# Performance work log

Measured on AMD Instinct MI355X. Metric: run time of the kernel, lower is better.

## Reference

```python
import jax, jax.numpy as jnp
import numpy as np

B, C, T = 16, 512, 1024
C8 = C // 8


def setup_inputs() -> dict:
    key = jax.random.key(0)
    ks = jax.random.split(key, 8)
    s_in = 1.0 / np.sqrt(C)  # torch Conv1d default init scale (fan_in = C*1)
    x = jax.random.normal(ks[0], (B, C, T), dtype=jnp.float32)
    q_w = jax.random.uniform(ks[1], (C8, C), jnp.float32, -s_in, s_in)
    q_b = jax.random.uniform(ks[2], (C8,), jnp.float32, -s_in, s_in)
    k_w = jax.random.uniform(ks[3], (C8, C), jnp.float32, -s_in, s_in)
    k_b = jax.random.uniform(ks[4], (C8,), jnp.float32, -s_in, s_in)
    v_w = jax.random.uniform(ks[5], (C, C), jnp.float32, -s_in, s_in)
    v_b = jax.random.uniform(ks[6], (C,), jnp.float32, -s_in, s_in)
    # gamma is nn.Parameter(torch.zeros(1)) at init; use a nonzero value so the
    # attention branch actually contributes to the output/gradients.
    gamma = jnp.full((1,), 0.5, dtype=jnp.float32)
    return {"x": x, "q_w": q_w, "q_b": q_b, "k_w": k_w, "k_b": k_b,
            "v_w": v_w, "v_b": v_b, "gamma": gamma}


def reference(x, q_w, q_b, k_w, k_b, v_w, v_b, gamma):
    # 1x1 Conv1d == per-timestep linear: weight [out, in]
    q = jnp.einsum('bct,dc->btd', x, q_w) + q_b              # [B, T, C/8]
    k = jnp.einsum('bct,dc->bdt', x, k_w) + k_b[:, None]     # [B, C/8, T]
    energy = jnp.einsum('btd,bds->bts', q, k)                # [B, T, T]
    attn = jax.nn.softmax(energy, axis=-1)                   # softmax over keys s
    v = jnp.einsum('bct,dc->bdt', x, v_w) + v_b[:, None]     # [B, C, T]
    # out[b,c,t] = sum_s v[b,c,s] * attn[b,t,s]
    out = jnp.einsum('bcs,bts->bct', v, attn)                # [B, C, T]
    return gamma * out + x
```

## Files before the change

### kernel.cpp

```cpp
#include <hip/hip_runtime.h>
#include <math.h>

constexpr int Bc = 16;
constexpr int Cc = 512;
constexpr int Tc = 1024;

typedef unsigned short u16;
typedef __attribute__((ext_vector_type(8))) short bf16x8;
typedef __attribute__((ext_vector_type(4))) float floatx4;

__device__ inline u16 f2bf(float f) {
    union { float f; unsigned u; } v; v.f = f;
    unsigned r = v.u + 0x7FFFu + ((v.u >> 16) & 1u);
    return (u16)(r >> 16);
}

__device__ inline void async16(const void* g, void* l) {
    __builtin_amdgcn_global_load_lds(
        (const __attribute__((address_space(1))) unsigned*)g,
        (__attribute__((address_space(3))) unsigned*)l, 16, 0, 0);
}

__global__ __launch_bounds__(256) void wconv_kernel(
    const float* __restrict__ qw, const float* __restrict__ kw,
    const float* __restrict__ vw, u16* __restrict__ wb)
{
    int i4 = blockIdx.x * 256 + threadIdx.x;
    int e  = i4 * 4;
    int row = e >> 9, col = e & 511;
    const float* src = (row < 64)  ? qw + (size_t)row * 512 + col
                     : (row < 128) ? kw + (size_t)(row - 64) * 512 + col
                                   : vw + (size_t)(row - 128) * 512 + col;
    float4 v = *(const float4*)src;
    ushort4 o = { f2bf(v.x), f2bf(v.y), f2bf(v.z), f2bf(v.w) };
    *(ushort4*)(wb + e) = o;
}

__global__ __launch_bounds__(256) void xtrans_kernel(
    const float* __restrict__ x, u16* __restrict__ xt)
{
    const int b = blockIdx.z, c0 = blockIdx.y * 64, t0 = blockIdx.x * 64;
    const int tid = threadIdx.x;
    __shared__ float xs[64][65];

    const float* xb = x + ((size_t)(b * Cc + c0)) * Tc + t0;
    #pragma unroll
    for (int r = 0; r < 4; ++r) {
        int f = tid + 256 * r;
        int c = f >> 4, tf = f & 15;
        float4 v = *(const float4*)(xb + (size_t)c * Tc + tf * 4);
        xs[c][tf * 4 + 0] = v.x; xs[c][tf * 4 + 1] = v.y;
        xs[c][tf * 4 + 2] = v.z; xs[c][tf * 4 + 3] = v.w;
    }
    __syncthreads();
    u16* xo = xt + ((size_t)b * Tc + t0) * Cc + c0;
    #pragma unroll
    for (int r = 0; r < 4; ++r) {
        int t  = (tid >> 4) + 16 * r;
        int cc = tid & 15;
        ushort4 o;
        o.x = f2bf(xs[cc * 4 + 0][t]); o.y = f2bf(xs[cc * 4 + 1][t]);
        o.z = f2bf(xs[cc * 4 + 2][t]); o.w = f2bf(xs[cc * 4 + 3][t]);
        *(ushort4*)(xo + (size_t)t * Cc + cc * 4) = o;
    }
}

__global__ __launch_bounds__(256, 2) void proj_kernel(
    const u16* __restrict__ wb, const u16* __restrict__ xt,
    const float* __restrict__ qb, const float* __restrict__ kb,
    const float* __restrict__ vb,
    u16* __restrict__ qt, u16* __restrict__ kt, u16* __restrict__ vc)
{
    const int b   = blockIdx.z;
    const int t0  = blockIdx.x * 128;
    const int n0  = blockIdx.y * 128;
    const int tid = threadIdx.x;
    const int w = tid >> 6, lane = tid & 63;
    const int l15 = lane & 15, q = lane >> 4;
    const int r8 = lane >> 3, h = lane & 7;
    const int nh = w >> 1, th = w & 1;

    __shared__ u16 As[128 * 64];
    __shared__ u16 Bs[128 * 64];

    floatx4 acc[4][4];
    #pragma unroll
    for (int i = 0; i < 4; ++i)
        #pragma unroll
        for (int j = 0; j < 4; ++j) acc[i][j] = (floatx4){0.f, 0.f, 0.f, 0.f};

    const u16* wbase = wb + (size_t)n0 * Cc;
    const u16* xbase = xt + ((size_t)b * Tc + t0) * Cc;

    for (int k0 = 0; k0 < Cc; k0 += 64) {
        #pragma unroll
        for (int i = 0; i < 4; ++i) {
            int row  = w * 32 + i * 8 + r8;
            int gcol = k0 + (((h + row) & 7) << 3);
            async16(wbase + (size_t)row * Cc + gcol, &As[(w * 32 + i * 8) * 64]);
            async16(xbase + (size_t)row * Cc + gcol, &Bs[(w * 32 + i * 8) * 64]);
        }
        asm volatile("s_waitcnt vmcnt(0)" ::: "memory");
        __syncthreads();

        #pragma unroll
        for (int ko = 0; ko < 64; ko += 32) {
            bf16x8 af[4], bf[4];
            const int cc = (ko >> 3) + q;
            #pragma unroll
            for (int i = 0; i < 4; ++i) {
                int row = nh * 64 + i * 16 + l15;
                af[i] = *(const bf16x8*)&As[row * 64 + (((cc - row) & 7) << 3)];
            }
            #pragma unroll
            for (int j = 0; j < 4; ++j) {
                int row = th * 64 + j * 16 + l15;
                bf[j] = *(const bf16x8*)&Bs[row * 64 + (((cc - row) & 7) << 3)];
            }
            #pragma unroll
            for (int i = 0; i < 4; ++i)
                #pragma unroll
                for (int j = 0; j < 4; ++j)
                    acc[i][j] = __builtin_amdgcn_mfma_f32_16x16x32_bf16(
                        af[i], bf[j], acc[i][j], 0, 0, 0);
        }
        __syncthreads();
    }

    if (n0 >= 128) {
        const int c_base = n0 - 128 + nh * 64;
        u16* vbb = vc + (size_t)b * Cc * Tc;
        #pragma unroll
        for (int i = 0; i < 4; ++i) {
            #pragma unroll
            for (int rr = 0; rr < 4; ++rr) {
                int c = c_base + i * 16 + q * 4 + rr;
                float bias = vb[c];
                #pragma unroll
                for (int j = 0; j < 4; ++j) {
                    int t = t0 + th * 64 + j * 16 + l15;
                    vbb[((size_t)c << 10) + t] = f2bf(acc[i][j][rr] + bias);
                }
            }
        }
    } else {
        const float* bias_p = nh ? kb : qb;
        u16* dst = nh ? kt : qt;
        u16* reg = ((w & 2) ? Bs : As) + (w & 1) * 4096;
        #pragma unroll
        for (int jh = 0; jh < 2; ++jh) {
            #pragma unroll
            for (int j2 = 0; j2 < 2; ++j2) {
                int j = jh * 2 + j2;
                int t_loc = j2 * 16 + l15;
                #pragma unroll
                for (int i = 0; i < 4; ++i) {
                    ushort4 o;
                    float b0 = bias_p[i * 16 + q * 4 + 0];
                    float b1 = bias_p[i * 16 + q * 4 + 1];
                    float b2 = bias_p[i * 16 + q * 4 + 2];
                    float b3 = bias_p[i * 16 + q * 4 + 3];
                    o.x = f2bf(acc[i][j][0] + b0);
                    o.y = f2bf(acc[i][j][1] + b1);
                    o.z = f2bf(acc[i][j][2] + b2);
                    o.w = f2bf(acc[i][j][3] + b3);
                    *(ushort4*)&reg[t_loc * 72 + i * 16 + q * 4] = o;
                }
            }
            const int cc8 = lane & 7, tb = lane >> 3;
            #pragma unroll
            for (int rr2 = 0; rr2 < 4; ++rr2) {
                int t32 = tb * 4 + rr2;
                bf16x8 vv = *(const bf16x8*)&reg[t32 * 72 + cc8 * 8];
                int t = t0 + th * 64 + jh * 32 + t32;
                *(bf16x8*)(dst + ((size_t)b * Tc + t) * 64 + cc8 * 8) = vv;
            }
            __builtin_amdgcn_wave_barrier();
        }
    }
}

__global__ __launch_bounds__(256, 2) void attn_kernel(
    const float* __restrict__ x,
    const u16* __restrict__ qt, const u16* __restrict__ kt,
    const u16* __restrict__ vc, const float* __restrict__ gp,
    float* __restrict__ out)
{
    const int tid = threadIdx.x, lane = tid & 63, w = tid >> 6;
    const int l15 = lane & 15, q = lane >> 4;
    const int l    = blockIdx.x;
    const int xcd  = l & 7, slot = l >> 3;
    const int combo = xcd * 4 + (slot >> 4);
    const int bx = slot & 15;
    const int b  = combo >> 1;
    const int by = combo & 1;
    const int t0 = bx * 64;
    const int cb = by * 256;

    __shared__ u16   P[2][4][16][40];
    __shared__ float lrow[64];
    __shared__ float tr2[4][16][68];

    const u16* qp = qt + ((size_t)b * Tc + t0 + w * 16 + l15) * 64 + q * 8;
    const bf16x8 qf0 = *(const bf16x8*)qp;
    const bf16x8 qf1 = *(const bf16x8*)(qp + 32);

    const u16* ktb = kt + (size_t)b * Tc * 64;
    const u16* vbb = vc + ((size_t)(b * Cc + cb + w * 64)) * Tc;

    floatx4 acc[4][4];
    #pragma unroll
    for (int i = 0; i < 4; ++i)
        #pragma unroll
        for (int j = 0; j < 4; ++j) acc[i][j] = (floatx4){0.f, 0.f, 0.f, 0.f};
    float lsum = 0.f;

    int buf = 0;
    #pragma unroll 1
    for (int s0 = 0; s0 < Tc; s0 += 32, buf ^= 1) {
        const u16* kp = ktb + (size_t)(s0 + l15) * 64 + q * 8;
        bf16x8 k00 = *(const bf16x8*)kp;
        bf16x8 k01 = *(const bf16x8*)(kp + 32);
        bf16x8 k10 = *(const bf16x8*)(kp + 1024);
        bf16x8 k11 = *(const bf16x8*)(kp + 1024 + 32);

        bf16x8 vf[4];
        const u16* vp = vbb + (size_t)l15 * Tc + s0 + q * 8;
        #pragma unroll
        for (int cg = 0; cg < 4; ++cg)
            vf[cg] = *(const bf16x8*)(vp + (size_t)cg * 16 * Tc);

        floatx4 e0 = (floatx4){0.f, 0.f, 0.f, 0.f};
        floatx4 e1 = (floatx4){0.f, 0.f, 0.f, 0.f};
        e0 = __builtin_amdgcn_mfma_f32_16x16x32_bf16(k00, qf0, e0, 0, 0, 0);
        e0 = __builtin_amdgcn_mfma_f32_16x16x32_bf16(k01, qf1, e0, 0, 0, 0);
        e1 = __builtin_amdgcn_mfma_f32_16x16x32_bf16(k10, qf0, e1, 0, 0, 0);
        e1 = __builtin_amdgcn_mfma_f32_16x16x32_bf16(k11, qf1, e1, 0, 0, 0);

        float p0[4], p1[4];
        #pragma unroll
        for (int r = 0; r < 4; ++r) { p0[r] = __expf(e0[r]); p1[r] = __expf(e1[r]); }
        lsum += p0[0] + p0[1] + p0[2] + p0[3] + p1[0] + p1[1] + p1[2] + p1[3];

        ushort4 w0 = { f2bf(p0[0]), f2bf(p0[1]), f2bf(p0[2]), f2bf(p0[3]) };
        ushort4 w1 = { f2bf(p1[0]), f2bf(p1[1]), f2bf(p1[2]), f2bf(p1[3]) };
        *(ushort4*)&P[buf][w][l15][q * 4]      = w0;
        *(ushort4*)&P[buf][w][l15][16 + q * 4] = w1;
        __syncthreads();

        #pragma unroll
        for (int tt = 0; tt < 4; ++tt) {
            bf16x8 pf = *(const bf16x8*)&P[buf][tt][l15][q * 8];
            #pragma unroll
            for (int cg = 0; cg < 4; ++cg)
                acc[tt][cg] = __builtin_amdgcn_mfma_f32_16x16x32_bf16(
                    pf, vf[cg], acc[tt][cg], 0, 0, 0);
        }
    }

    lsum += __shfl_xor(lsum, 16);
    lsum += __shfl_xor(lsum, 32);
    if (lane < 16) lrow[w * 16 + lane] = lsum;
    __syncthreads();

    const float g = gp[0];
    float sc[4][4];
    #pragma unroll
    for (int tt = 0; tt < 4; ++tt)
        #pragma unroll
        for (int rr = 0; rr < 4; ++rr)
            sc[tt][rr] = g / lrow[tt * 16 + q * 4 + rr];

    const float* xb = x   + ((size_t)(b * Cc + cb + w * 64)) * Tc + t0;
    float*       ob = out + ((size_t)(b * Cc + cb + w * 64)) * Tc + t0;
    #pragma unroll
    for (int cg = 0; cg < 4; ++cg) {
        #pragma unroll
        for (int tt = 0; tt < 4; ++tt) {
            float4 vv;
            vv.x = acc[tt][cg][0] * sc[tt][0];
            vv.y = acc[tt][cg][1] * sc[tt][1];
            vv.z = acc[tt][cg][2] * sc[tt][2];
            vv.w = acc[tt][cg][3] * sc[tt][3];
            *(float4*)&tr2[w][l15][tt * 16 + q * 4] = vv;
        }
        #pragma unroll
        for (int i = 0; i < 4; ++i) {
            int cr = i * 4 + (lane >> 4);
            int t4 = (lane & 15) * 4;
            float4 vv = *(const float4*)&tr2[w][cr][t4];
            size_t go = (size_t)(cg * 16 + cr) * Tc + t4;
            float4 xv = *(const float4*)(xb + go);
            vv.x += xv.x; vv.y += xv.y; vv.z += xv.z; vv.w += xv.w;
            *(float4*)(ob + go) = vv;
        }
        __builtin_amdgcn_wave_barrier();
    }
}

extern "C" void kernel_launch(void* const* d_in, const int* in_sizes, int n_in,
                              void* d_out, int out_size, void* d_ws, size_t ws_size,
                              hipStream_t stream) {
    const float* x     = (const float*)d_in[0];
    const float* qw    = (const float*)d_in[1];
    const float* qbias = (const float*)d_in[2];
    const float* kw    = (const float*)d_in[3];
    const float* kbias = (const float*)d_in[4];
    const float* vw    = (const float*)d_in[5];
    const float* vbias = (const float*)d_in[6];
    const float* gamma = (const float*)d_in[7];
    float* out = (float*)d_out;

    u16* wb = (u16*)d_ws;
    u16* xt = wb + (size_t)640 * 512;
    u16* qt = xt + (size_t)Bc * Tc * Cc;
    u16* kt = qt + (size_t)Bc * Tc * 64;
    u16* vc = kt + (size_t)Bc * Tc * 64;

    wconv_kernel<<<320, 256, 0, stream>>>(qw, kw, vw, wb);
    xtrans_kernel<<<dim3(Tc / 64, Cc / 64, Bc), 256, 0, stream>>>(x, xt);
    proj_kernel<<<dim3(Tc / 128, 5, Bc), 256, 0, stream>>>(
        wb, xt, qbias, kbias, vbias, qt, kt, vc);
    attn_kernel<<<dim3(512), 256, 0, stream>>>(
        x, qt, kt, vc, gamma, out);
}
```

Before: 178.5 us.

## Split attention channels into four groups and fold log2e into Q for exp2

The attention kernel now splits the 512 channels into four groups of 128 instead of two of 256. That doubles the grid to 1024 blocks, halves each wave's accumulators and V loads, and raises the occupancy hint to 3 blocks per CU. The Q projection is prescaled by log2(e) so the softmax can use the hardware exp2, and the probabilities are packed into bf16 pairs with a permute instruction. In exchange, the QK^T energy and exp work is recomputed twice as often across channel groups. The new packing rounds differently from the previous round-to-nearest-even.

```diff
diff --git a/kernel.cpp b/kernel.cpp
--- a/kernel.cpp
+++ b/kernel.cpp
@@ -6,13 +6,25 @@
 constexpr int Tc = 1024;
 
 typedef unsigned short u16;
+typedef unsigned int u32;
 typedef __attribute__((ext_vector_type(8))) short bf16x8;
 typedef __attribute__((ext_vector_type(4))) float floatx4;
+
+#if __has_builtin(__builtin_amdgcn_exp2f)
+#define EXP2F(x) __builtin_amdgcn_exp2f(x)
+#else
+#define EXP2F(x) __expf((x) * 0.6931471805599453f)
+#endif
 
 __device__ inline u16 f2bf(float f) {
     union { float f; unsigned u; } v; v.f = f;
     unsigned r = v.u + 0x7FFFu + ((v.u >> 16) & 1u);
     return (u16)(r >> 16);
+}
+
+__device__ inline u32 pkbf(float a, float b) {
+    union { float f; u32 u; } ua, ub; ua.f = a; ub.f = b;
+    return __builtin_amdgcn_perm(ub.u + 0x8000u, ua.u + 0x8000u, 0x07060302u);
 }
 
 __device__ inline void async16(const void* g, void* l) {
@@ -144,6 +156,7 @@
             }
         }
     } else {
+        const float qsc = nh ? 1.0f : 1.44269504088896f;
         const float* bias_p = nh ? kb : qb;
         u16* dst = nh ? kt : qt;
         u16* reg = ((w & 2) ? Bs : As) + (w & 1) * 4096;
@@ -160,10 +173,10 @@
                     float b1 = bias_p[i * 16 + q * 4 + 1];
                     float b2 = bias_p[i * 16 + q * 4 + 2];
                     float b3 = bias_p[i * 16 + q * 4 + 3];
-                    o.x = f2bf(acc[i][j][0] + b0);
-                    o.y = f2bf(acc[i][j][1] + b1);
-                    o.z = f2bf(acc[i][j][2] + b2);
-                    o.w = f2bf(acc[i][j][3] + b3);
+                    o.x = f2bf((acc[i][j][0] + b0) * qsc);
+                    o.y = f2bf((acc[i][j][1] + b1) * qsc);
+                    o.z = f2bf((acc[i][j][2] + b2) * qsc);
+                    o.w = f2bf((acc[i][j][3] + b3) * qsc);
                     *(ushort4*)&reg[t_loc * 72 + i * 16 + q * 4] = o;
                 }
             }
@@ -180,7 +193,7 @@
     }
 }
 
-__global__ __launch_bounds__(256, 2) void attn_kernel(
+__global__ __launch_bounds__(256, 3) void attn_kernel(
     const float* __restrict__ x,
     const u16* __restrict__ qt, const u16* __restrict__ kt,
     const u16* __restrict__ vc, const float* __restrict__ gp,
@@ -188,14 +201,14 @@
 {
     const int tid = threadIdx.x, lane = tid & 63, w = tid >> 6;
     const int l15 = lane & 15, q = lane >> 4;
-    const int l    = blockIdx.x;
-    const int xcd  = l & 7, slot = l >> 3;
-    const int combo = xcd * 4 + (slot >> 4);
+    const int l     = blockIdx.x;
+    const int xcd   = l & 7, slot = l >> 3;
+    const int combo = xcd * 8 + (slot >> 4);
     const int bx = slot & 15;
-    const int b  = combo >> 1;
-    const int by = combo & 1;
+    const int b  = combo >> 2;
+    const int by = combo & 3;
     const int t0 = bx * 64;
-    const int cb = by * 256;
+    const int cb = by * 128;
 
     __shared__ u16   P[2][4][16][40];
     __shared__ float lrow[64];
@@ -206,13 +219,13 @@
     const bf16x8 qf1 = *(const bf16x8*)(qp + 32);
 
     const u16* ktb = kt + (size_t)b * Tc * 64;
-    const u16* vbb = vc + ((size_t)(b * Cc + cb + w * 64)) * Tc;
-
-    floatx4 acc[4][4];
+    const u16* vbb = vc + ((size_t)(b * Cc + cb + w * 32)) * Tc;
+
+    floatx4 acc[4][2];
     #pragma unroll
     for (int i = 0; i < 4; ++i)
         #pragma unroll
-        for (int j = 0; j < 4; ++j) acc[i][j] = (floatx4){0.f, 0.f, 0.f, 0.f};
+        for (int j = 0; j < 2; ++j) acc[i][j] = (floatx4){0.f, 0.f, 0.f, 0.f};
     float lsum = 0.f;
 
     int buf = 0;
@@ -224,11 +237,10 @@
         bf16x8 k10 = *(const bf16x8*)(kp + 1024);
         bf16x8 k11 = *(const bf16x8*)(kp + 1024 + 32);
 
-        bf16x8 vf[4];
+        bf16x8 vf[2];
         const u16* vp = vbb + (size_t)l15 * Tc + s0 + q * 8;
-        #pragma unroll
-        for (int cg = 0; cg < 4; ++cg)
-            vf[cg] = *(const bf16x8*)(vp + (size_t)cg * 16 * Tc);
+        vf[0] = *(const bf16x8*)(vp);
+        vf[1] = *(const bf16x8*)(vp + (size_t)16 * Tc);
 
         floatx4 e0 = (floatx4){0.f, 0.f, 0.f, 0.f};
         floatx4 e1 = (floatx4){0.f, 0.f, 0.f, 0.f};
@@ -239,22 +251,23 @@
 
         float p0[4], p1[4];
         #pragma unroll
-        for (int r = 0; r < 4; ++r) { p0[r] = __expf(e0[r]); p1[r] = __expf(e1[r]); }
-        lsum += p0[0] + p0[1] + p0[2] + p0[3] + p1[0] + p1[1] + p1[2] + p1[3];
-
-        ushort4 w0 = { f2bf(p0[0]), f2bf(p0[1]), f2bf(p0[2]), f2bf(p0[3]) };
-        ushort4 w1 = { f2bf(p1[0]), f2bf(p1[1]), f2bf(p1[2]), f2bf(p1[3]) };
-        *(ushort4*)&P[buf][w][l15][q * 4]      = w0;
-        *(ushort4*)&P[buf][w][l15][16 + q * 4] = w1;
+        for (int r = 0; r < 4; ++r) { p0[r] = EXP2F(e0[r]); p1[r] = EXP2F(e1[r]); }
+        lsum += ((p0[0] + p0[1]) + (p0[2] + p0[3]))
+              + ((p1[0] + p1[1]) + (p1[2] + p1[3]));
+
+        uint2 w0 = { pkbf(p0[0], p0[1]), pkbf(p0[2], p0[3]) };
+        uint2 w1 = { pkbf(p1[0], p1[1]), pkbf(p1[2], p1[3]) };
+        *(uint2*)&P[buf][w][l15][q * 4]      = w0;
+        *(uint2*)&P[buf][w][l15][16 + q * 4] = w1;
         __syncthreads();
 
         #pragma unroll
         for (int tt = 0; tt < 4; ++tt) {
             bf16x8 pf = *(const bf16x8*)&P[buf][tt][l15][q * 8];
-            #pragma unroll
-            for (int cg = 0; cg < 4; ++cg)
-                acc[tt][cg] = __builtin_amdgcn_mfma_f32_16x16x32_bf16(
-                    pf, vf[cg], acc[tt][cg], 0, 0, 0);
+            acc[tt][0] = __builtin_amdgcn_mfma_f32_16x16x32_bf16(
+                pf, vf[0], acc[tt][0], 0, 0, 0);
+            acc[tt][1] = __builtin_amdgcn_mfma_f32_16x16x32_bf16(
+                pf, vf[1], acc[tt][1], 0, 0, 0);
         }
     }
 
@@ -271,10 +284,10 @@
         for (int rr = 0; rr < 4; ++rr)
             sc[tt][rr] = g / lrow[tt * 16 + q * 4 + rr];
 
-    const float* xb = x   + ((size_t)(b * Cc + cb + w * 64)) * Tc + t0;
-    float*       ob = out + ((size_t)(b * Cc + cb + w * 64)) * Tc + t0;
-    #pragma unroll
-    for (int cg = 0; cg < 4; ++cg) {
+    const float* xb = x   + ((size_t)(b * Cc + cb + w * 32)) * Tc + t0;
+    float*       ob = out + ((size_t)(b * Cc + cb + w * 32)) * Tc + t0;
+    #pragma unroll
+    for (int cg = 0; cg < 2; ++cg) {
         #pragma unroll
         for (int tt = 0; tt < 4; ++tt) {
             float4 vv;
@@ -321,6 +334,6 @@
     xtrans_kernel<<<dim3(Tc / 64, Cc / 64, Bc), 256, 0, stream>>>(x, xt);
     proj_kernel<<<dim3(Tc / 128, 5, Bc), 256, 0, stream>>>(
         wb, xt, qbias, kbias, vbias, qt, kt, vc);
-    attn_kernel<<<dim3(512), 256, 0, stream>>>(
+    attn_kernel<<<dim3(1024), 256, 0, stream>>>(
         x, qt, kt, vc, gamma, out);
 }
```

Result: slower. 207.4 us (+16.2%).
